# Performance work log

Measured on AMD Instinct MI355X. Metric: run time of the kernel, lower is better.

## Reference

```python
import jax, jax.numpy as jnp
import numpy as np

N = 100000   # num_nodes (also in_channels of layer 1, since x=None)
R = 50       # num_relations
B = 30       # num_bases
H = 16       # hidden channels
C = 8        # num_classes
E = 1600000  # num_edges (avg degree 16)


def setup_inputs() -> dict:
    key = jax.random.key(0)
    ks = jax.random.split(key, 10)
    s = 0.05
    edge_index = jax.random.randint(ks[0], (2, E), 0, N, dtype=jnp.int32)
    edge_type = jax.random.randint(ks[1], (E,), 0, R, dtype=jnp.int32)
    # layer 1 (in=N because x is None -> node-index / embedding mode)
    basis1 = jax.random.normal(ks[2], (B, N, H), jnp.float32) * s
    comp1 = jax.random.normal(ks[3], (R, B), jnp.float32) * s
    root1 = jax.random.normal(ks[4], (N, H), jnp.float32) * s
    bias1 = jnp.zeros((H,), jnp.float32)
    # layer 2 (in=H, out=C)
    basis2 = jax.random.normal(ks[5], (B, H, C), jnp.float32) * s
    comp2 = jax.random.normal(ks[6], (R, B), jnp.float32) * s
    root2 = jax.random.normal(ks[7], (H, C), jnp.float32) * s
    bias2 = jnp.zeros((C,), jnp.float32)
    return dict(edge_index=edge_index, edge_type=edge_type,
                basis1=basis1, comp1=comp1, root1=root1, bias1=bias1,
                basis2=basis2, comp2=comp2, root2=root2, bias2=bias2)


def reference(edge_index, edge_type, basis1, comp1, root1, bias1,
              basis2, comp2, root2, bias2):
    src, dst = edge_index[0], edge_index[1]
    # PyG RGCNConv uses aggr='mean' per relation: each message is divided by
    # the number of same-relation incoming edges at its target node.
    seg = dst * R + edge_type                                   # [E] (node, rel) segment id
    cnt = jax.ops.segment_sum(jnp.ones((E,), jnp.float32), seg, num_segments=N * R)
    inv = 1.0 / jnp.maximum(cnt, 1.0)                           # [N*R]
    inv_e = inv[seg][:, None]                                   # [E,1]

    # ---- layer 1: x = None -> message_e = weight[rel_e][src_e] ----
    w1 = jnp.einsum('rb,bnh->rnh', comp1, basis1)               # [R,N,H] basis-combined weights
    msg1 = w1[edge_type, src] * inv_e                           # [E,H]
    h = jax.ops.segment_sum(msg1, dst, num_segments=N)          # [N,H]
    h = h + root1 + bias1                                       # root embedding + bias
    # NOTE: source does `x.relu()` without assignment -> no-op; faithfully omitted.

    # ---- layer 2: mean-aggregate per (node, relation), then per-relation matmul ----
    w2 = jnp.einsum('rb,bhc->rhc', comp2, basis2)               # [R,H,C]
    agg = jax.ops.segment_sum(h[src] * inv_e, seg, num_segments=N * R)
    agg = agg.reshape(N, R, H)                                  # [N,R,H]
    out = jnp.einsum('nrh,rhc->nc', agg, w2) + h @ root2 + bias2
    return out
```

## Files before the change

### kernel.cpp

```cpp
#include <hip/hip_runtime.h>

#define NREL   50
#define NBASE  30
#define HID    16
#define NCLS   8

#define SHIFT   9
#define BWID    (1 << SHIFT)
#define NBUKMAX 512
#define TILE    4096
#define EPB     16
#define W2T     56
#define C1P     36

typedef float    vf4 __attribute__((ext_vector_type(4)));
typedef _Float16 vh8 __attribute__((ext_vector_type(8)));


__global__ void compute_w2_kernel(const float* __restrict__ comp2,
                                  const float* __restrict__ basis2,
                                  float* __restrict__ w2) {
    int i = blockIdx.x * blockDim.x + threadIdx.x;
    if (i >= NREL * HID * NCLS) return;
    int r  = i / (HID * NCLS);
    int hc = i % (HID * NCLS);
    float acc = 0.f;
    #pragma unroll
    for (int b = 0; b < NBASE; ++b)
        acc += comp2[r * NBASE + b] * basis2[b * HID * NCLS + hc];
    w2[i] = acc;
}


__global__ void ghist_kernel(const int* __restrict__ src,
                             const int* __restrict__ dst,
                             int* __restrict__ hs, int* __restrict__ hd,
                             int E, int nbuk) {
    __shared__ int lhs[NBUKMAX], lhd[NBUKMAX];
    for (int j = threadIdx.x; j < nbuk; j += blockDim.x) { lhs[j] = 0; lhd[j] = 0; }
    __syncthreads();
    for (long e = (long)blockIdx.x * blockDim.x + threadIdx.x; e < E;
         e += (long)gridDim.x * blockDim.x) {
        atomicAdd(&lhs[src[e] >> SHIFT], 1);
        atomicAdd(&lhd[dst[e] >> SHIFT], 1);
    }
    __syncthreads();
    for (int j = threadIdx.x; j < nbuk; j += blockDim.x) {
        if (lhs[j]) atomicAdd(&hs[j], lhs[j]);
        if (lhd[j]) atomicAdd(&hd[j], lhd[j]);
    }
}

__global__ void scanbuk_kernel(const int* __restrict__ hs, const int* __restrict__ hd,
                               int* __restrict__ gcs, int* __restrict__ bases_s,
                               int* __restrict__ based, int* __restrict__ gcd,
                               int nbuk, int E) {
    __shared__ int a[NBUKMAX], b[NBUKMAX];
    int tid = threadIdx.x;
    for (int j = tid; j < nbuk; j += blockDim.x) { a[j] = hs[j]; b[j] = hd[j]; }
    __syncthreads();
    if (tid == 0) {
        int run = 0;
        for (int i = 0; i < nbuk; ++i) { int v = a[i]; a[i] = run; run += v; }
        run = 0;
        for (int i = 0; i < nbuk; ++i) { int v = b[i]; b[i] = run; run += v; }
    }
    __syncthreads();
    for (int j = tid; j < nbuk; j += blockDim.x) {
        gcs[j] = a[j]; bases_s[j] = a[j];
        based[j] = b[j]; gcd[j] = b[j];
    }
    if (tid == 0) { bases_s[nbuk] = E; based[nbuk] = E; }
}

__global__ void pass1_kernel(const int* __restrict__ src,
                             const int* __restrict__ dst,
                             const int* __restrict__ et,
                             int* __restrict__ gcur,
                             int* __restrict__ Ax0, int* __restrict__ Ad0, int E) {
    __shared__ int lhist[NBUKMAX], lbase[NBUKMAX], lcur[NBUKMAX];
    int tid = threadIdx.x;
    for (int j = tid; j < NBUKMAX; j += 256) { lhist[j] = 0; lcur[j] = 0; }
    __syncthreads();
    int px[EPB], pd[EPB]; int bk[EPB];
    long e0 = (long)blockIdx.x * TILE;
    #pragma unroll
    for (int j = 0; j < EPB; ++j) {
        long e = e0 + j * 256 + tid;
        if (e < E) {
            int s = src[e], d = dst[e], t = et[e];
            px[j] = s | (t << 17);
            pd[j] = d;
            bk[j] = s >> SHIFT;
            atomicAdd(&lhist[bk[j]], 1);
        } else bk[j] = -1;
    }
    __syncthreads();
    for (int j = tid; j < NBUKMAX; j += 256)
        if (lhist[j] > 0) lbase[j] = atomicAdd(&gcur[j], lhist[j]);
    __syncthreads();
    #pragma unroll
    for (int j = 0; j < EPB; ++j) {
        if (bk[j] >= 0) {
            int r = atomicAdd(&lcur[bk[j]], 1);
            int pos = lbase[bk[j]] + r;
            Ax0[pos] = px[j];
            Ad0[pos] = pd[j];
        }
    }
}

__global__ void pass1b_kernel(const int* __restrict__ Ax0,
                              const int* __restrict__ Ad0,
                              const int* __restrict__ bases_s,
                              int* __restrict__ Ax, int* __restrict__ Ad,
                              int* __restrict__ rowptr_s, int N, int E) {
    __shared__ int lh[BWID], sA[BWID], sB[BWID];
    int blk = blockIdx.x, tid = threadIdx.x;
    int k0 = bases_s[blk], k1 = bases_s[blk + 1], cnt = k1 - k0;
    for (int j = tid; j < BWID; j += 256) lh[j] = 0;
    __syncthreads();
    for (int i = tid; i < cnt; i += 256) {
        int slow = Ax0[k0 + i] & (BWID - 1);
        atomicAdd(&lh[slow], 1);
    }
    __syncthreads();
    for (int j = tid; j < BWID; j += 256) sA[j] = lh[j];
    __syncthreads();
    int* cur = sA; int* oth = sB;
    for (int off = 1; off < BWID; off <<= 1) {
        for (int j = tid; j < BWID; j += 256)
            oth[j] = cur[j] + (j >= off ? cur[j - off] : 0);
        __syncthreads();
        int* t_ = cur; cur = oth; oth = t_;
    }
    for (int j = tid; j < BWID; j += 256) {
        int excl = cur[j] - lh[j];
        oth[j] = excl;
        int s = blk * BWID + j;
        if (s < N) rowptr_s[s] = k0 + excl;
    }
    __syncthreads();
    for (int i = tid; i < cnt; i += 256) {
        int x = Ax0[k0 + i], d = Ad0[k0 + i];
        int slow = x & (BWID - 1);
        int pos = atomicAdd(&oth[slow], 1);
        Ax[k0 + pos] = x;
        Ad[k0 + pos] = d;
    }
    if (blk == 0 && tid == 0) rowptr_s[N] = E;
}

__global__ void pass2_kernel(const int* __restrict__ Ax,
                             const int* __restrict__ Ad,
                             int* __restrict__ gcur, int2* __restrict__ B, int E) {
    __shared__ int lhist[NBUKMAX], lbase[NBUKMAX], lcur[NBUKMAX];
    int tid = threadIdx.x;
    for (int j = tid; j < NBUKMAX; j += 256) { lhist[j] = 0; lcur[j] = 0; }
    __syncthreads();
    int2 p[EPB]; int bk[EPB];
    long e0 = (long)blockIdx.x * TILE;
    #pragma unroll
    for (int j = 0; j < EPB; ++j) {
        long e = e0 + j * 256 + tid;
        if (e < E) {
            int x = Ax[e];
            int d = Ad[e];
            p[j] = make_int2(x, (int)e | ((d & (BWID - 1)) << 21));
            bk[j] = d >> SHIFT;
            atomicAdd(&lhist[bk[j]], 1);
        } else bk[j] = -1;
    }
    __syncthreads();
    for (int j = tid; j < NBUKMAX; j += 256)
        if (lhist[j] > 0) lbase[j] = atomicAdd(&gcur[j], lhist[j]);
    __syncthreads();
    #pragma unroll
    for (int j = 0; j < EPB; ++j) {
        if (bk[j] >= 0) {
            int r = atomicAdd(&lcur[bk[j]], 1);
            B[lbase[bk[j]] + r] = p[j];
        }
    }
}

__global__ void pass3_kernel(const int2* __restrict__ B,
                             const int* __restrict__ based,
                             int2* __restrict__ e2, int* __restrict__ rowptr,
                             int N, int E) {
    __shared__ int lh[BWID], sA[BWID], sB[BWID];
    int blk = blockIdx.x, tid = threadIdx.x;
    int k0 = based[blk], k1 = based[blk + 1], cnt = k1 - k0;
    for (int j = tid; j < BWID; j += 256) lh[j] = 0;
    __syncthreads();
    for (int i = tid; i < cnt; i += 256) {
        int dlow = ((unsigned)B[k0 + i].y) >> 21;
        atomicAdd(&lh[dlow], 1);
    }
    __syncthreads();
    for (int j = tid; j < BWID; j += 256) sA[j] = lh[j];
    __syncthreads();
    int* cur = sA; int* oth = sB;
    for (int off = 1; off < BWID; off <<= 1) {
        for (int j = tid; j < BWID; j += 256)
            oth[j] = cur[j] + (j >= off ? cur[j - off] : 0);
        __syncthreads();
        int* t_ = cur; cur = oth; oth = t_;
    }
    for (int j = tid; j < BWID; j += 256) {
        int excl = cur[j] - lh[j];
        oth[j] = excl;
        int d = blk * BWID + j;
        if (d < N) rowptr[d] = k0 + excl;
    }
    __syncthreads();
    for (int i = tid; i < cnt; i += 256) {
        int2 b = B[k0 + i];
        int dlow = ((unsigned)b.y) >> 21;
        int pos = atomicAdd(&oth[dlow], 1);
        e2[k0 + pos] = make_int2(b.x, b.y & 0x1FFFFF);
    }
    if (blk == 0 && tid == 0) rowptr[N] = E;
}

__global__ void layer1A_node_kernel(const int* __restrict__ Ax,
                                    const int* __restrict__ rowptr_s,
                                    const float* __restrict__ comp1,
                                    const float* __restrict__ basis1,
                                    _Float16* __restrict__ msg, int N) {
    __shared__ float c1s[NREL * C1P];
    for (int i = threadIdx.x; i < NREL * C1P; i += blockDim.x) {
        int t = i / C1P, b = i % C1P;
        c1s[i] = (b < NBASE) ? comp1[t * NBASE + b] : 0.f;
    }
    __syncthreads();
    int gid = threadIdx.x >> 4;
    int l   = threadIdx.x & 15;
    int s = blockIdx.x * 16 + gid;
    if (s >= N) return;
    int k0 = rowptr_s[s], k1 = rowptr_s[s + 1];
    if (k0 == k1) return;

    vf4 b4[8];
    {
        long stride = (long)N * HID;
        const float* bp = basis1 + (long)s * HID + l;
        float breg[32];
        #pragma unroll
        for (int b = 0; b < NBASE; ++b)
            breg[b] = bp[(long)b * stride];
        #pragma unroll
        for (int b = NBASE; b < 32; ++b) breg[b] = 0.f;
        #pragma unroll
        for (int i = 0; i < 8; ++i)
            b4[i] = (vf4){breg[4*i], breg[4*i+1], breg[4*i+2], breg[4*i+3]};
    }

    int k = k0;
    for (; k + 4 <= k1; k += 4) {
        int t0 = ((unsigned)Ax[k + 0]) >> 17;
        int t1 = ((unsigned)Ax[k + 1]) >> 17;
        int t2 = ((unsigned)Ax[k + 2]) >> 17;
        int t3 = ((unsigned)Ax[k + 3]) >> 17;
        const vf4* c0 = reinterpret_cast<const vf4*>(c1s + t0 * C1P);
        const vf4* c1 = reinterpret_cast<const vf4*>(c1s + t1 * C1P);
        const vf4* c2 = reinterpret_cast<const vf4*>(c1s + t2 * C1P);
        const vf4* c3 = reinterpret_cast<const vf4*>(c1s + t3 * C1P);
        vf4 a0 = {0.f,0.f,0.f,0.f}, a1 = a0, a2 = a0, a3 = a0;
        #pragma unroll
        for (int i = 0; i < 8; ++i) {
            a0 += c0[i] * b4[i];
            a1 += c1[i] * b4[i];
            a2 += c2[i] * b4[i];
            a3 += c3[i] * b4[i];
        }
        float r0 = (a0.x + a0.y) + (a0.z + a0.w);
        float r1 = (a1.x + a1.y) + (a1.z + a1.w);
        float r2 = (a2.x + a2.y) + (a2.z + a2.w);
        float r3 = (a3.x + a3.y) + (a3.z + a3.w);
        __builtin_nontemporal_store((_Float16)r0, &msg[(long)(k + 0) * HID + l]);
        __builtin_nontemporal_store((_Float16)r1, &msg[(long)(k + 1) * HID + l]);
        __builtin_nontemporal_store((_Float16)r2, &msg[(long)(k + 2) * HID + l]);
        __builtin_nontemporal_store((_Float16)r3, &msg[(long)(k + 3) * HID + l]);
    }
    for (; k < k1; ++k) {
        int t = ((unsigned)Ax[k]) >> 17;
        const vf4* cr4 = reinterpret_cast<const vf4*>(c1s + t * C1P);
        vf4 acc4 = {0.f, 0.f, 0.f, 0.f};
        #pragma unroll
        for (int i = 0; i < 8; ++i)
            acc4 += cr4[i] * b4[i];
        float acc = (acc4.x + acc4.y) + (acc4.z + acc4.w);
        __builtin_nontemporal_store((_Float16)acc, &msg[(long)k * HID + l]);
    }
}

__global__ void layer1B_kernel(const int2* __restrict__ e2,
                               const int* __restrict__ rowptr,
                               const _Float16* __restrict__ msg,
                               const float* __restrict__ root1,
                               const float* __restrict__ bias1,
                               float* __restrict__ h, float* __restrict__ sinv, int N) {
    long gid = (long)blockIdx.x * blockDim.x + threadIdx.x;
    int d = (int)(gid >> 3);
    if (d >= N) return;
    int q = (int)(gid & 7);
    int k0 = rowptr[d], k1 = rowptr[d + 1];

    float acc[HID];
    #pragma unroll
    for (int i = 0; i < HID; ++i) acc[i] = 0.f;

    for (int k = k0 + q; k < k1; k += 8) {
        int2 v = e2[k];
        unsigned t = ((unsigned)v.x) >> 17;
        int c = 0;
        for (int j = k0; j < k1; ++j)
            c += ((((unsigned)e2[j].x) >> 17) == t);
        float inv = 1.0f / (float)c;
        sinv[k] = inv;
        const vh8* m8 = reinterpret_cast<const vh8*>(msg + (long)v.y * HID);
        vh8 m0 = __builtin_nontemporal_load(m8);
        vh8 m1 = __builtin_nontemporal_load(m8 + 1);
        #pragma unroll
        for (int i = 0; i < 8; ++i) {
            acc[i]     += inv * (float)m0[i];
            acc[i + 8] += inv * (float)m1[i];
        }
    }

    #pragma unroll
    for (int i = 0; i < HID; ++i) {
        acc[i] += __shfl_xor(acc[i], 1);
        acc[i] += __shfl_xor(acc[i], 2);
        acc[i] += __shfl_xor(acc[i], 4);
    }

    if (q == 0) {
        float4* h4 = reinterpret_cast<float4*>(h + (size_t)d * HID);
        #pragma unroll
        for (int p = 0; p < HID / 4; ++p) {
            float4 r = *reinterpret_cast<const float4*>(root1 + (size_t)d * HID + p * 4);
            float4 bv = *reinterpret_cast<const float4*>(bias1 + p * 4);
            h4[p] = make_float4(acc[4 * p + 0] + r.x + bv.x,
                                acc[4 * p + 1] + r.y + bv.y,
                                acc[4 * p + 2] + r.z + bv.z,
                                acc[4 * p + 3] + r.w + bv.w);
        }
    }
}

__global__ void layer2_kernel(const int2* __restrict__ e2,
                              const int* __restrict__ rowptr,
                              const float* __restrict__ sinv,
                              const float* __restrict__ w2,
                              const float* __restrict__ h,
                              const float* __restrict__ root2,
                              const float* __restrict__ bias2,
                              float* __restrict__ out, int N) {
    __shared__ float w2s[HID * NCLS * W2T];
    for (int i = threadIdx.x; i < NREL * HID * NCLS; i += blockDim.x) {
        int t = i / (HID * NCLS);
        int hc = i % (HID * NCLS);
        w2s[hc * W2T + t] = w2[i];
    }
    __syncthreads();

    int gid = blockIdx.x * blockDim.x + threadIdx.x;
    int d = gid >> 2;
    if (d >= N) return;
    int q = gid & 3;
    int k0 = rowptr[d], k1 = rowptr[d + 1];

    float acc[NCLS];
    #pragma unroll
    for (int c = 0; c < NCLS; ++c) acc[c] = 0.f;

    for (int k = k0 + q; k < k1; k += 4) {
        int2 v = e2[k];
        int s = v.x & 0x1FFFF;
        int t = ((unsigned)v.x) >> 17;
        float inv = sinv[k];
        const float4* h4 = reinterpret_cast<const float4*>(h + (size_t)s * HID);
        float tmp[NCLS];
        #pragma unroll
        for (int c = 0; c < NCLS; ++c) tmp[c] = 0.f;
        #pragma unroll
        for (int p = 0; p < HID / 4; ++p) {
            float4 hv = h4[p];
            float hvv[4] = {hv.x, hv.y, hv.z, hv.w};
            #pragma unroll
            for (int j = 0; j < 4; ++j) {
                int i = 4 * p + j;
                #pragma unroll
                for (int c = 0; c < NCLS; ++c)
                    tmp[c] += hvv[j] * w2s[(i * NCLS + c) * W2T + t];
            }
        }
        #pragma unroll
        for (int c = 0; c < NCLS; ++c) acc[c] += inv * tmp[c];
    }

    #pragma unroll
    for (int c = 0; c < NCLS; ++c) {
        acc[c] += __shfl_xor(acc[c], 1);
        acc[c] += __shfl_xor(acc[c], 2);
    }

    if (q == 0) {
        const float4* h4 = reinterpret_cast<const float4*>(h + (size_t)d * HID);
        #pragma unroll
        for (int p = 0; p < HID / 4; ++p) {
            float4 hv = h4[p];
            float hvv[4] = {hv.x, hv.y, hv.z, hv.w};
            #pragma unroll
            for (int j = 0; j < 4; ++j) {
                int i = 4 * p + j;
                #pragma unroll
                for (int c = 0; c < NCLS; ++c)
                    acc[c] += hvv[j] * root2[i * NCLS + c];
            }
        }
        #pragma unroll
        for (int c = 0; c < NCLS; ++c) acc[c] += bias2[c];
        float4* o4 = reinterpret_cast<float4*>(out + (size_t)d * NCLS);
        o4[0] = make_float4(acc[0], acc[1], acc[2], acc[3]);
        o4[1] = make_float4(acc[4], acc[5], acc[6], acc[7]);
    }
}


extern "C" void kernel_launch(void* const* d_in, const int* in_sizes, int n_in,
                              void* d_out, int out_size, void* d_ws, size_t ws_size,
                              hipStream_t stream) {
    const int*   edge_index = (const int*)  d_in[0];
    const int*   edge_type  = (const int*)  d_in[1];
    const float* basis1     = (const float*)d_in[2];
    const float* comp1      = (const float*)d_in[3];
    const float* root1      = (const float*)d_in[4];
    const float* bias1      = (const float*)d_in[5];
    const float* basis2     = (const float*)d_in[6];
    const float* comp2      = (const float*)d_in[7];
    const float* root2      = (const float*)d_in[8];
    const float* bias2      = (const float*)d_in[9];
    float* out = (float*)d_out;

    const int E = in_sizes[1];
    const int N = in_sizes[4] / HID;
    const int nbuk = (N + BWID - 1) >> SHIFT;
    const int* src = edge_index;
    const int* dst = edge_index + E;

    char* base = (char*)d_ws;
    size_t off = 0;
    auto alloc = [&](size_t bytes, size_t align) -> char* {
        off = (off + align - 1) & ~(align - 1);
        char* p = base + off;
        off += bytes;
        return p;
    };
    int*  hs       = (int*)  alloc((size_t)NBUKMAX * 4, 4);
    int*  hd       = (int*)  alloc((size_t)NBUKMAX * 4, 4);
    int*  gcs      = (int*)  alloc((size_t)NBUKMAX * 4, 4);
    int*  gcd      = (int*)  alloc((size_t)NBUKMAX * 4, 4);
    int*  bases_s  = (int*)  alloc((size_t)(NBUKMAX + 1) * 4, 4);
    int*  based    = (int*)  alloc((size_t)(NBUKMAX + 1) * 4, 4);
    int*  rowptr   = (int*)  alloc((size_t)(N + 1) * 4, 4);
    int*  rowptr_s = (int*)  alloc((size_t)(N + 1) * 4, 4);
    float* w2      = (float*)alloc((size_t)NREL * HID * NCLS * 4, 16);
    float* h       = (float*)alloc((size_t)N * HID * 4, 16);
    float* sinv    = (float*)alloc((size_t)E * 4, 4);
    int*  Ax0      = (int*)  alloc((size_t)E * 4, 4);
    int*  Ad0      = (int*)  alloc((size_t)E * 4, 4);
    int*  Ax       = (int*)  alloc((size_t)E * 4, 4);
    int*  Ad       = (int*)  alloc((size_t)E * 4, 4);
    int2* B        = (int2*) alloc((size_t)E * 8, 8);
    int2* e2       = (int2*) alloc((size_t)E * 8, 8);
    _Float16* msg  = (_Float16*)alloc((size_t)E * HID * 2, 16);

    hipMemsetAsync(hs, 0, (size_t)NBUKMAX * 2 * 4, stream);

    {   int M = NREL * HID * NCLS;
        compute_w2_kernel<<<(M + 255) / 256, 256, 0, stream>>>(comp2, basis2, w2);
    }
    ghist_kernel<<<2048, 256, 0, stream>>>(src, dst, hs, hd, E, nbuk);
    scanbuk_kernel<<<1, 256, 0, stream>>>(hs, hd, gcs, bases_s, based, gcd, nbuk, E);

    int nblk = (E + TILE - 1) / TILE;
    pass1_kernel<<<nblk, 256, 0, stream>>>(src, dst, edge_type, gcs, Ax0, Ad0, E);
    pass1b_kernel<<<nbuk, 256, 0, stream>>>(Ax0, Ad0, bases_s, Ax, Ad, rowptr_s, N, E);
    pass2_kernel<<<nblk, 256, 0, stream>>>(Ax, Ad, gcd, B, E);
    pass3_kernel<<<nbuk, 256, 0, stream>>>(B, based, e2, rowptr, N, E);

    {   long total = (long)N * 16;
        int blocks = (int)((N + 15) / 16);
        layer1A_node_kernel<<<blocks, 256, 0, stream>>>(
            Ax, rowptr_s, comp1, basis1, msg, N);
        (void)total;
    }
    {   long total = (long)N * 8;
        layer1B_kernel<<<(int)((total + 255) / 256), 256, 0, stream>>>(
            e2, rowptr, msg, root1, bias1, h, sinv, N);
    }
    {   long total = (long)N * 4;
        layer2_kernel<<<(int)((total + 255) / 256), 256, 0, stream>>>(
            e2, rowptr, sinv, w2, h, root2, bias2, out, N);
    }
}
```

Measured before the change: 380.5 us.

## Store hidden h in fp16, widen layer2 to 8 lanes, prefetch edge keys

Changes the intermediate hidden features h from fp32 to fp16, halving the bytes gathered per edge in layer2 and written by layer1B. Layer2 now uses 8 threads per destination node instead of 4, with an extra shuffle step in the reduction. The layer1A inner loop is software-pipelined so the next four edge keys are loaded before the current four are computed. The fp16 h adds rounding error to layer 2 inputs and the root term, and doubling layer2's thread count also doubles its blocks and the per-block shared-memory w2 staging.

```diff
diff --git a/kernel.cpp b/kernel.cpp
--- a/kernel.cpp
+++ b/kernel.cpp
@@ -257,31 +257,38 @@
     }
 
     int k = k0;
-    for (; k + 4 <= k1; k += 4) {
-        int t0 = ((unsigned)Ax[k + 0]) >> 17;
-        int t1 = ((unsigned)Ax[k + 1]) >> 17;
-        int t2 = ((unsigned)Ax[k + 2]) >> 17;
-        int t3 = ((unsigned)Ax[k + 3]) >> 17;
-        const vf4* c0 = reinterpret_cast<const vf4*>(c1s + t0 * C1P);
-        const vf4* c1 = reinterpret_cast<const vf4*>(c1s + t1 * C1P);
-        const vf4* c2 = reinterpret_cast<const vf4*>(c1s + t2 * C1P);
-        const vf4* c3 = reinterpret_cast<const vf4*>(c1s + t3 * C1P);
-        vf4 a0 = {0.f,0.f,0.f,0.f}, a1 = a0, a2 = a0, a3 = a0;
-        #pragma unroll
-        for (int i = 0; i < 8; ++i) {
-            a0 += c0[i] * b4[i];
-            a1 += c1[i] * b4[i];
-            a2 += c2[i] * b4[i];
-            a3 += c3[i] * b4[i];
-        }
-        float r0 = (a0.x + a0.y) + (a0.z + a0.w);
-        float r1 = (a1.x + a1.y) + (a1.z + a1.w);
-        float r2 = (a2.x + a2.y) + (a2.z + a2.w);
-        float r3 = (a3.x + a3.y) + (a3.z + a3.w);
-        __builtin_nontemporal_store((_Float16)r0, &msg[(long)(k + 0) * HID + l]);
-        __builtin_nontemporal_store((_Float16)r1, &msg[(long)(k + 1) * HID + l]);
-        __builtin_nontemporal_store((_Float16)r2, &msg[(long)(k + 2) * HID + l]);
-        __builtin_nontemporal_store((_Float16)r3, &msg[(long)(k + 3) * HID + l]);
+    if (k + 4 <= k1) {
+        int c0x = Ax[k + 0], c1x = Ax[k + 1], c2x = Ax[k + 2], c3x = Ax[k + 3];
+        for (;;) {
+            bool more = (k + 8 <= k1);
+            int n0, n1, n2, n3;
+            if (more) {
+                n0 = Ax[k + 4]; n1 = Ax[k + 5]; n2 = Ax[k + 6]; n3 = Ax[k + 7];
+            }
+            const vf4* c0 = reinterpret_cast<const vf4*>(c1s + (((unsigned)c0x) >> 17) * C1P);
+            const vf4* c1 = reinterpret_cast<const vf4*>(c1s + (((unsigned)c1x) >> 17) * C1P);
+            const vf4* c2 = reinterpret_cast<const vf4*>(c1s + (((unsigned)c2x) >> 17) * C1P);
+            const vf4* c3 = reinterpret_cast<const vf4*>(c1s + (((unsigned)c3x) >> 17) * C1P);
+            vf4 a0 = {0.f,0.f,0.f,0.f}, a1 = a0, a2 = a0, a3 = a0;
+            #pragma unroll
+            for (int i = 0; i < 8; ++i) {
+                a0 += c0[i] * b4[i];
+                a1 += c1[i] * b4[i];
+                a2 += c2[i] * b4[i];
+                a3 += c3[i] * b4[i];
+            }
+            float r0 = (a0.x + a0.y) + (a0.z + a0.w);
+            float r1 = (a1.x + a1.y) + (a1.z + a1.w);
+            float r2 = (a2.x + a2.y) + (a2.z + a2.w);
+            float r3 = (a3.x + a3.y) + (a3.z + a3.w);
+            __builtin_nontemporal_store((_Float16)r0, &msg[(long)(k + 0) * HID + l]);
+            __builtin_nontemporal_store((_Float16)r1, &msg[(long)(k + 1) * HID + l]);
+            __builtin_nontemporal_store((_Float16)r2, &msg[(long)(k + 2) * HID + l]);
+            __builtin_nontemporal_store((_Float16)r3, &msg[(long)(k + 3) * HID + l]);
+            k += 4;
+            if (!more) break;
+            c0x = n0; c1x = n1; c2x = n2; c3x = n3;
+        }
     }
     for (; k < k1; ++k) {
         int t = ((unsigned)Ax[k]) >> 17;
@@ -300,7 +307,7 @@
                                const _Float16* __restrict__ msg,
                                const float* __restrict__ root1,
                                const float* __restrict__ bias1,
-                               float* __restrict__ h, float* __restrict__ sinv, int N) {
+                               _Float16* __restrict__ h, float* __restrict__ sinv, int N) {
     long gid = (long)blockIdx.x * blockDim.x + threadIdx.x;
     int d = (int)(gid >> 3);
     if (d >= N) return;
@@ -337,16 +344,15 @@
     }
 
     if (q == 0) {
-        float4* h4 = reinterpret_cast<float4*>(h + (size_t)d * HID);
-        #pragma unroll
-        for (int p = 0; p < HID / 4; ++p) {
-            float4 r = *reinterpret_cast<const float4*>(root1 + (size_t)d * HID + p * 4);
-            float4 bv = *reinterpret_cast<const float4*>(bias1 + p * 4);
-            h4[p] = make_float4(acc[4 * p + 0] + r.x + bv.x,
-                                acc[4 * p + 1] + r.y + bv.y,
-                                acc[4 * p + 2] + r.z + bv.z,
-                                acc[4 * p + 3] + r.w + bv.w);
-        }
+        vh8 o0, o1;
+        #pragma unroll
+        for (int i = 0; i < 8; ++i) {
+            o0[i] = (_Float16)(acc[i]     + root1[(size_t)d * HID + i]     + bias1[i]);
+            o1[i] = (_Float16)(acc[i + 8] + root1[(size_t)d * HID + i + 8] + bias1[i + 8]);
+        }
+        vh8* h8 = reinterpret_cast<vh8*>(h + (size_t)d * HID);
+        h8[0] = o0;
+        h8[1] = o1;
     }
 }
 
@@ -354,7 +360,7 @@
                               const int* __restrict__ rowptr,
                               const float* __restrict__ sinv,
                               const float* __restrict__ w2,
-                              const float* __restrict__ h,
+                              const _Float16* __restrict__ h,
                               const float* __restrict__ root2,
                               const float* __restrict__ bias2,
                               float* __restrict__ out, int N) {
@@ -366,36 +372,35 @@
     }
     __syncthreads();
 
-    int gid = blockIdx.x * blockDim.x + threadIdx.x;
-    int d = gid >> 2;
+    long gid = (long)blockIdx.x * blockDim.x + threadIdx.x;
+    int d = (int)(gid >> 3);
     if (d >= N) return;
-    int q = gid & 3;
+    int q = (int)(gid & 7);
     int k0 = rowptr[d], k1 = rowptr[d + 1];
 
     float acc[NCLS];
     #pragma unroll
     for (int c = 0; c < NCLS; ++c) acc[c] = 0.f;
 
-    for (int k = k0 + q; k < k1; k += 4) {
+    for (int k = k0 + q; k < k1; k += 8) {
         int2 v = e2[k];
         int s = v.x & 0x1FFFF;
         int t = ((unsigned)v.x) >> 17;
         float inv = sinv[k];
-        const float4* h4 = reinterpret_cast<const float4*>(h + (size_t)s * HID);
+        const vh8* h8 = reinterpret_cast<const vh8*>(h + (size_t)s * HID);
+        vh8 m0 = h8[0];
+        vh8 m1 = h8[1];
+        float hv[HID];
+        #pragma unroll
+        for (int i = 0; i < 8; ++i) { hv[i] = (float)m0[i]; hv[i + 8] = (float)m1[i]; }
         float tmp[NCLS];
         #pragma unroll
         for (int c = 0; c < NCLS; ++c) tmp[c] = 0.f;
         #pragma unroll
-        for (int p = 0; p < HID / 4; ++p) {
-            float4 hv = h4[p];
-            float hvv[4] = {hv.x, hv.y, hv.z, hv.w};
+        for (int i = 0; i < HID; ++i) {
             #pragma unroll
-            for (int j = 0; j < 4; ++j) {
-                int i = 4 * p + j;
-                #pragma unroll
-                for (int c = 0; c < NCLS; ++c)
-                    tmp[c] += hvv[j] * w2s[(i * NCLS + c) * W2T + t];
-            }
+            for (int c = 0; c < NCLS; ++c)
+                tmp[c] += hv[i] * w2s[(i * NCLS + c) * W2T + t];
         }
         #pragma unroll
         for (int c = 0; c < NCLS; ++c) acc[c] += inv * tmp[c];
@@ -405,21 +410,21 @@
     for (int c = 0; c < NCLS; ++c) {
         acc[c] += __shfl_xor(acc[c], 1);
         acc[c] += __shfl_xor(acc[c], 2);
+        acc[c] += __shfl_xor(acc[c], 4);
     }
 
     if (q == 0) {
-        const float4* h4 = reinterpret_cast<const float4*>(h + (size_t)d * HID);
-        #pragma unroll
-        for (int p = 0; p < HID / 4; ++p) {
-            float4 hv = h4[p];
-            float hvv[4] = {hv.x, hv.y, hv.z, hv.w};
+        const vh8* h8 = reinterpret_cast<const vh8*>(h + (size_t)d * HID);
+        vh8 m0 = h8[0];
+        vh8 m1 = h8[1];
+        float hv[HID];
+        #pragma unroll
+        for (int i = 0; i < 8; ++i) { hv[i] = (float)m0[i]; hv[i + 8] = (float)m1[i]; }
+        #pragma unroll
+        for (int i = 0; i < HID; ++i) {
             #pragma unroll
-            for (int j = 0; j < 4; ++j) {
-                int i = 4 * p + j;
-                #pragma unroll
-                for (int c = 0; c < NCLS; ++c)
-                    acc[c] += hvv[j] * root2[i * NCLS + c];
-            }
+            for (int c = 0; c < NCLS; ++c)
+                acc[c] += hv[i] * root2[i * NCLS + c];
         }
         #pragma unroll
         for (int c = 0; c < NCLS; ++c) acc[c] += bias2[c];
@@ -468,7 +473,7 @@
     int*  rowptr   = (int*)  alloc((size_t)(N + 1) * 4, 4);
     int*  rowptr_s = (int*)  alloc((size_t)(N + 1) * 4, 4);
     float* w2      = (float*)alloc((size_t)NREL * HID * NCLS * 4, 16);
-    float* h       = (float*)alloc((size_t)N * HID * 4, 16);
+    _Float16* h    = (_Float16*)alloc((size_t)N * HID * 2, 16);
     float* sinv    = (float*)alloc((size_t)E * 4, 4);
     int*  Ax0      = (int*)  alloc((size_t)E * 4, 4);
     int*  Ad0      = (int*)  alloc((size_t)E * 4, 4);
@@ -492,17 +497,15 @@
     pass2_kernel<<<nblk, 256, 0, stream>>>(Ax, Ad, gcd, B, E);
     pass3_kernel<<<nbuk, 256, 0, stream>>>(B, based, e2, rowptr, N, E);
 
-    {   long total = (long)N * 16;
-        int blocks = (int)((N + 15) / 16);
+    {   int blocks = (int)((N + 15) / 16);
         layer1A_node_kernel<<<blocks, 256, 0, stream>>>(
             Ax, rowptr_s, comp1, basis1, msg, N);
-        (void)total;
     }
     {   long total = (long)N * 8;
         layer1B_kernel<<<(int)((total + 255) / 256), 256, 0, stream>>>(
             e2, rowptr, msg, root1, bias1, h, sinv, N);
     }
-    {   long total = (long)N * 4;
+    {   long total = (long)N * 8;
         layer2_kernel<<<(int)((total + 255) / 256), 256, 0, stream>>>(
             e2, rowptr, sinv, w2, h, root2, bias2, out, N);
     }
```

Measured after the change: 377.2 us. About the same (-0.9%).
